# Optimization experiments

Measured on AMD Instinct MI355X. Metric: run time of the kernel, lower is better.

Reference implementation:

```python
import jax, jax.numpy as jnp
import numpy as np

B, S, D = 4, 4096, 1024
H = 8                    # num_heads
DK = D // H              # head_k_dim = 128
DV = D // H              # head_v_dim = 128
KLEPE = 5                # lepe kernel size
ROPE_BASE = 10000.0


def rotate_half(x):
    x1, x2 = jnp.split(x, 2, axis=-1)
    return jnp.concatenate([-x2, x1], axis=-1)


def rope_sin_cos(seq_len, dim):
    inv_freq = 1.0 / (ROPE_BASE ** (jnp.arange(0, dim, 2, dtype=jnp.float32) / dim))
    freqs = jnp.arange(seq_len, dtype=jnp.float32)[:, None] * inv_freq[None, :]
    emb = jnp.concatenate([freqs, freqs], axis=-1)  # [S, dim]
    return jnp.sin(emb), jnp.cos(emb)


def mala_attn(q, k, v):
    """Magnitude-aware linear attention with inline RoPE.

    Attention weights A_ij = (scale*q_i.k_j + 1) / (scale*q_i.(sum_j k_j) + S):
    rows sum to 1 but, unlike plain linear attention, the sharpness of the
    distribution still depends on ||q_i|| (magnitude rectification). Computed
    in O(S*d^2) linear form without materializing the SxS matrix.
    q, k: [B,S,H,DK]; v: [B,S,H,DV].
    """
    sin, cos = rope_sin_cos(q.shape[1], q.shape[-1])
    sin, cos = sin[None, :, None, :], cos[None, :, None, :]
    q = q * cos + rotate_half(q) * sin
    k = k * cos + rotate_half(k) * sin
    scale = q.shape[-1] ** -0.5
    seq_len = q.shape[1]
    kv = jnp.einsum('bshd,bshe->bhde', k, v)      # [B,H,DK,DV]
    ksum = k.sum(axis=1)                          # [B,H,DK]
    vsum = v.sum(axis=1)                          # [B,H,DV]
    num = jnp.einsum('bshd,bhde->bshe', q, kv) * scale + vsum[:, None, :, :]
    den = jnp.einsum('bshd,bhd->bsh', q, ksum) * scale + seq_len
    return num / den[..., None]


def lepe_conv(v, w, b):
    # depthwise Conv1d over the sequence axis; channel id = h*DV + d
    Bb, Ss = v.shape[0], v.shape[1]
    x = v.transpose(0, 2, 3, 1).reshape(Bb, H * DV, Ss)   # [B, C, S]
    y = jax.lax.conv_general_dilated(
        x, w, window_strides=(1,), padding=[(KLEPE // 2, KLEPE // 2)],
        dimension_numbers=('NCH', 'OIH', 'NCH'), feature_group_count=H * DV)
    y = y + b[None, :, None]
    return y.reshape(Bb, H, DV, Ss).transpose(0, 3, 1, 2)  # [B,S,H,DV]


def setup_inputs() -> dict:
    key = jax.random.key(0)
    ks = jax.random.split(key, 8)
    w = 0.02
    return {
        'hidden_states': jax.random.normal(ks[0], (B, S, D), dtype=jnp.float32),
        'Wq': jax.random.normal(ks[1], (D, D), dtype=jnp.float32) * w,
        'Wk': jax.random.normal(ks[2], (D, D), dtype=jnp.float32) * w,
        'Wv': jax.random.normal(ks[3], (D, D), dtype=jnp.float32) * w,
        'Wg': jax.random.normal(ks[4], (D, D), dtype=jnp.float32) * w,
        'Wo': jax.random.normal(ks[5], (D, D), dtype=jnp.float32) * w,
        'lepe_w': jax.random.normal(ks[6], (D, 1, KLEPE), dtype=jnp.float32) * 0.1,
        'lepe_b': jnp.zeros((D,), dtype=jnp.float32),
    }


def reference(hidden_states, Wq, Wk, Wv, Wg, Wo, lepe_w, lepe_b):
    Bb, Ss, _ = hidden_states.shape
    q = (hidden_states @ Wq.T).reshape(Bb, Ss, H, DK)
    k = (hidden_states @ Wk.T).reshape(Bb, Ss, H, DK)
    v = (hidden_states @ Wv.T).reshape(Bb, Ss, H, DV)
    o_gate = hidden_states @ Wg.T                          # [B,S,D]
    o = mala_attn(q, k, v) + lepe_conv(v, lepe_w, lepe_b)  # [B,S,H,DV]
    o = o.reshape(Bb, Ss, H * DV) * o_gate
    return o @ Wo.T
```

## Files before the change

kernel.cpp:

```cpp
#include <hip/hip_runtime.h>
#include <math.h>
#include <stdint.h>


typedef __bf16 bf16;
typedef __bf16 bf16x2 __attribute__((ext_vector_type(2)));
typedef __bf16 bf16x4 __attribute__((ext_vector_type(4)));
typedef __bf16 bf16x8 __attribute__((ext_vector_type(8)));
typedef float f32x4 __attribute__((ext_vector_type(4)));

static constexpr float kScale = 0.08838834764831845f;

__device__ __forceinline__ void async_copy16(const void* g, void* l) {
  __builtin_amdgcn_global_load_lds(
      (const __attribute__((address_space(1))) void*)(uintptr_t)g,
      (__attribute__((address_space(3))) void*)(uintptr_t)l, 16, 0, 0);
}

__global__ __launch_bounds__(512, 1) void gemm_qkvg(
    const bf16* __restrict__ A, const bf16* __restrict__ Bw,
    bf16* __restrict__ C, const float2* __restrict__ tab)
{
  __shared__ __align__(16) char smem[131072];

  const int t = threadIdx.x;
  const int bid = blockIdx.x;
  const int n = bid >> 3;
  const int bx = (bid & 7) * 8 + (n & 7);
  const int by = n >> 3;
  const long m0 = (long)bx * 256;
  const long n0 = (long)by * 256;

  const int d0 = t * 16;
  const int dd = d0 ^ (((d0 >> 7) & 7) << 4);
  const int rT = dd >> 7;
  const int cT = (dd & 127) >> 1;
  const bf16* aSt = A  + (m0 + rT) * 1024 + cT;
  const bf16* bSt = Bw + (n0 + rT) * 1024 + cT;
  char* ldsDst = smem + d0;

  const int lane = t & 63, wid = t >> 6;
  const int wm = wid >> 2, wn = wid & 3;
  const int fm = lane & 15, fq = lane >> 4;
  const int xsw = (fm & 7) << 4;
  const int o0 = (fq * 16) ^ xsw;
  const int o1 = o0 ^ 64;
  const char* ldsA0 = smem + wm * 16384 + fm * 128 + o0;
  const char* ldsA1 = smem + wm * 16384 + fm * 128 + o1;
  const char* ldsB0 = smem + 32768 + (wn >> 1) * 16384 +
                      ((wn & 1) * 64 + fm) * 128 + o0;
  const char* ldsB1 = ldsB0 + (o1 - o0);

  f32x4 acc[8][4] = {};
  bf16x8 a4[4][2], b4[4][2];

#define STAGE_A(kt, h) do {                                                  \
    const bf16* s_ = aSt + (long)(h) * 131072 + (kt) * 64;                   \
    char* d_ = ldsDst + ((kt) & 1) * 65536 + (h) * 16384;                    \
    async_copy16(s_, d_);                                                    \
    async_copy16(s_ + 65536, d_ + 8192);                                     \
  } while (0)
#define STAGE_B(kt, h) do {                                                  \
    const bf16* s_ = bSt + (long)(h) * 131072 + (kt) * 64;                   \
    char* d_ = ldsDst + ((kt) & 1) * 65536 + 32768 + (h) * 16384;            \
    async_copy16(s_, d_);                                                    \
    async_copy16(s_ + 65536, d_ + 8192);                                     \
  } while (0)
#define LOAD_A(buf, qi) do {                                                 \
    const char* p0_ = ldsA0 + (buf) * 65536 + (qi) * 8192;                   \
    const char* p1_ = ldsA1 + (buf) * 65536 + (qi) * 8192;                   \
    a4[0][0] = *(const bf16x8*)(p0_);                                        \
    a4[0][1] = *(const bf16x8*)(p1_);                                        \
    a4[1][0] = *(const bf16x8*)(p0_ + 2048);                                 \
    a4[1][1] = *(const bf16x8*)(p1_ + 2048);                                 \
    a4[2][0] = *(const bf16x8*)(p0_ + 4096);                                 \
    a4[2][1] = *(const bf16x8*)(p1_ + 4096);                                 \
    a4[3][0] = *(const bf16x8*)(p0_ + 6144);                                 \
    a4[3][1] = *(const bf16x8*)(p1_ + 6144);                                 \
  } while (0)
#define LOAD_B(buf, qj) do {                                                 \
    const char* p0_ = ldsB0 + (buf) * 65536 + (qj) * 4096;                   \
    const char* p1_ = ldsB1 + (buf) * 65536 + (qj) * 4096;                   \
    b4[2*(qj)+0][0] = *(const bf16x8*)(p0_);                                 \
    b4[2*(qj)+0][1] = *(const bf16x8*)(p1_);                                 \
    b4[2*(qj)+1][0] = *(const bf16x8*)(p0_ + 2048);                          \
    b4[2*(qj)+1][1] = *(const bf16x8*)(p1_ + 2048);                          \
  } while (0)
#define MM1(i, j, ks)                                                        \
    acc[i][j] = __builtin_amdgcn_mfma_f32_16x16x32_bf16(                     \
        a4[(i) & 3][ks], b4[j][ks], acc[i][j], 0, 0, 0)
#define MFMA_Q(qi, qj) do {                                                  \
    MM1(4*(qi)+0, 2*(qj)+0, 0); MM1(4*(qi)+1, 2*(qj)+0, 0);                  \
    MM1(4*(qi)+2, 2*(qj)+0, 0); MM1(4*(qi)+3, 2*(qj)+0, 0);                  \
    MM1(4*(qi)+0, 2*(qj)+1, 0); MM1(4*(qi)+1, 2*(qj)+1, 0);                  \
    MM1(4*(qi)+2, 2*(qj)+1, 0); MM1(4*(qi)+3, 2*(qj)+1, 0);                  \
    MM1(4*(qi)+0, 2*(qj)+0, 1); MM1(4*(qi)+1, 2*(qj)+0, 1);                  \
    MM1(4*(qi)+2, 2*(qj)+0, 1); MM1(4*(qi)+3, 2*(qj)+0, 1);                  \
    MM1(4*(qi)+0, 2*(qj)+1, 1); MM1(4*(qi)+1, 2*(qj)+1, 1);                  \
    MM1(4*(qi)+2, 2*(qj)+1, 1); MM1(4*(qi)+3, 2*(qj)+1, 1);                  \
  } while (0)
#define BAR()    __builtin_amdgcn_s_barrier()
#define SCHEDB() __builtin_amdgcn_sched_barrier(0)
#define PRIO(p)  __builtin_amdgcn_s_setprio(p)

  STAGE_A(0, 0); STAGE_A(0, 1); STAGE_B(0, 0); STAGE_B(0, 1);
  STAGE_A(1, 0);
  asm volatile("s_waitcnt vmcnt(2)" ::: "memory");
  BAR(); SCHEDB();

#pragma unroll 1
  for (int it = 0; it < 7; ++it) {
    const int k1 = 2 * it + 1;
    const int k2 = 2 * it + 2;
    const int k3 = 2 * it + 3;
    LOAD_A(0, 0); LOAD_B(0, 0);
    STAGE_A(k1, 1);
    BAR(); SCHEDB(); PRIO(1); MFMA_Q(0, 0); PRIO(0); BAR(); SCHEDB();
    LOAD_B(0, 1);
    STAGE_B(k1, 0);
    BAR(); SCHEDB(); PRIO(1); MFMA_Q(0, 1); PRIO(0); BAR(); SCHEDB();
    LOAD_A(0, 1);
    STAGE_B(k1, 1);
    BAR(); SCHEDB(); PRIO(1); MFMA_Q(1, 1); PRIO(0); BAR(); SCHEDB();
    STAGE_A(k2, 0);
    BAR(); SCHEDB(); PRIO(1); MFMA_Q(1, 0); PRIO(0);
    asm volatile("s_waitcnt vmcnt(2)" ::: "memory");
    BAR(); SCHEDB();
    LOAD_A(1, 0); LOAD_B(1, 0);
    STAGE_A(k2, 1);
    BAR(); SCHEDB(); PRIO(1); MFMA_Q(0, 0); PRIO(0); BAR(); SCHEDB();
    LOAD_B(1, 1);
    STAGE_B(k2, 0);
    BAR(); SCHEDB(); PRIO(1); MFMA_Q(0, 1); PRIO(0); BAR(); SCHEDB();
    LOAD_A(1, 1);
    STAGE_B(k2, 1);
    BAR(); SCHEDB(); PRIO(1); MFMA_Q(1, 1); PRIO(0); BAR(); SCHEDB();
    STAGE_A(k3, 0);
    BAR(); SCHEDB(); PRIO(1); MFMA_Q(1, 0); PRIO(0);
    asm volatile("s_waitcnt vmcnt(2)" ::: "memory");
    BAR(); SCHEDB();
  }

  {
    LOAD_A(0, 0); LOAD_B(0, 0);
    STAGE_A(15, 1);
    BAR(); SCHEDB(); PRIO(1); MFMA_Q(0, 0); PRIO(0); BAR(); SCHEDB();
    LOAD_B(0, 1);
    STAGE_B(15, 0);
    BAR(); SCHEDB(); PRIO(1); MFMA_Q(0, 1); PRIO(0); BAR(); SCHEDB();
    LOAD_A(0, 1);
    STAGE_B(15, 1);
    BAR(); SCHEDB(); PRIO(1); MFMA_Q(1, 1); PRIO(0); BAR(); SCHEDB();
    BAR(); SCHEDB(); PRIO(1); MFMA_Q(1, 0); PRIO(0);
    asm volatile("s_waitcnt vmcnt(0)" ::: "memory");
    BAR(); SCHEDB();
    LOAD_A(1, 0); LOAD_B(1, 0);
    BAR(); SCHEDB(); PRIO(1); MFMA_Q(0, 0); PRIO(0); BAR(); SCHEDB();
    LOAD_B(1, 1);
    BAR(); SCHEDB(); PRIO(1); MFMA_Q(0, 1); PRIO(0); BAR(); SCHEDB();
    LOAD_A(1, 1);
    BAR(); SCHEDB(); PRIO(1); MFMA_Q(1, 1); PRIO(0); BAR(); SCHEDB();
    BAR(); SCHEDB(); PRIO(1); MFMA_Q(1, 0); PRIO(0); BAR(); SCHEDB();
  }

#undef STAGE_A
#undef STAGE_B
#undef LOAD_A
#undef LOAD_B
#undef MM1
#undef MFMA_Q
#undef BAR
#undef SCHEDB
#undef PRIO

  bf16* T = (bf16*)smem;
  __syncthreads();
#pragma unroll 1
  for (int hw = 0; hw < 2; ++hw) {
    if (wm == hw) {
#pragma unroll
      for (int rf = 0; rf < 8; ++rf)
#pragma unroll
        for (int cf = 0; cf < 4; ++cf)
#pragma unroll
          for (int r = 0; r < 4; ++r)
            T[(rf * 16 + fq * 4 + r) * 264 + wn * 64 + cf * 16 + fm] =
                (bf16)acc[rf][cf][r];
    }
    __syncthreads();
    if (by < 8) {
#pragma unroll
      for (int ii = 0; ii < 32; ++ii) {
        const int pi = t + ii * 512;
        const int row = pi >> 7, pr = pi & 127;
        const int hd = pr >> 6, i = pr & 63;
        const int c0 = hd * 128 + i;
        const int s = (int)((m0 + hw * 128 + row) & 4095);
        const float2 sc = tab[s * 64 + i];
        float x1 = (float)T[row * 264 + c0];
        float x2 = (float)T[row * 264 + c0 + 64];
        T[row * 264 + c0]      = (bf16)(x1 * sc.y - x2 * sc.x);
        T[row * 264 + c0 + 64] = (bf16)(x2 * sc.y + x1 * sc.x);
      }
      __syncthreads();
    }
#pragma unroll
    for (int ii = 0; ii < 8; ++ii) {
      const int cid = t + ii * 512;
      const int row = cid >> 5, ch = cid & 31;
      *(bf16x8*)(C + (m0 + hw * 128 + row) * 4096 + n0 + ch * 8) =
          *(const bf16x8*)(T + row * 264 + ch * 8);
    }
    __syncthreads();
  }
}

__global__ __launch_bounds__(256, 2) void gemm_final(
    const bf16* __restrict__ A, const bf16* __restrict__ Bw,
    float* __restrict__ C)
{
  __shared__ __align__(16) bf16 As[128 * 32];
  __shared__ __align__(16) bf16 Bs[128 * 32];
  const int t = threadIdx.x;
  const int bid = blockIdx.x;
  const int xcd = bid & 7, n = bid >> 3;
  const int bx = xcd * 16 + (n & 15);
  const int by = n >> 4;
  const long m0 = (long)bx * 128;
  A  += m0 * 1024;
  Bw += (long)by * 131072;
  C  += m0 * 1024 + (long)by * 128;

  const int i0 = t, i1 = t + 256;
  const bf16* gA0 = A  + (long)(i0 >> 2) * 1024 + (i0 & 3) * 8;
  const bf16* gA1 = A  + (long)(i1 >> 2) * 1024 + (i1 & 3) * 8;
  const bf16* gB0 = Bw + (long)(i0 >> 2) * 1024 + (i0 & 3) * 8;
  const bf16* gB1 = Bw + (long)(i1 >> 2) * 1024 + (i1 & 3) * 8;
  bf16* lA0 = As + i0 * 8; bf16* lA1 = As + i1 * 8;
  bf16* lB0 = Bs + i0 * 8; bf16* lB1 = Bs + i1 * 8;

  const int lane = t & 63, wv = t >> 6;
  const int moff = (wv & 1) * 64, noff = (wv >> 1) * 64;
  const int fm = lane & 15, fq = lane >> 4;

  f32x4 acc[4][4] = {};

  for (int k0 = 0; k0 < 1024; k0 += 32) {
    async_copy16(gA0, lA0); async_copy16(gA1, lA1);
    async_copy16(gB0, lB0); async_copy16(gB1, lB1);
    gA0 += 32; gA1 += 32; gB0 += 32; gB1 += 32;
    __syncthreads();
    bf16x8 af[4], bfv[4];
#pragma unroll
    for (int i = 0; i < 4; ++i) {
      af[i]  = *(const bf16x8*)(As + (moff + i * 16 + fm) * 32 + fq * 8);
      bfv[i] = *(const bf16x8*)(Bs + (noff + i * 16 + fm) * 32 + fq * 8);
    }
#pragma unroll
    for (int i = 0; i < 4; ++i)
#pragma unroll
      for (int j = 0; j < 4; ++j)
        acc[i][j] = __builtin_amdgcn_mfma_f32_16x16x32_bf16(af[i], bfv[j], acc[i][j], 0, 0, 0);
    __syncthreads();
  }

#pragma unroll
  for (int i = 0; i < 4; ++i)
#pragma unroll
    for (int j = 0; j < 4; ++j)
#pragma unroll
      for (int r = 0; r < 4; ++r)
        C[(long)(moff + i * 16 + fq * 4 + r) * 1024 + noff + j * 16 + fm] = acc[i][j][r];
}

__global__ __launch_bounds__(256, 2) void gemm_num(
    const bf16* __restrict__ QKVG, const bf16* __restrict__ kvTall,
    const float* __restrict__ ksum, const float* __restrict__ vsum,
    const float* __restrict__ lepe_w, const float* __restrict__ lepe_b,
    bf16* __restrict__ obuf)
{
  __shared__ __align__(16) char smem[17408];
  bf16* As = (bf16*)smem;
  bf16* Bs = (bf16*)(smem + 8192);
  bf16* T  = (bf16*)smem;
  __shared__ float sden[128], svsum[128], slb[128], sksum[128];
  __shared__ float slw[5][128];

  const int t = threadIdx.x;
  const int h = blockIdx.y, b = blockIdx.z;
  const int bh = b * 8 + h;
  const long m0 = (long)blockIdx.x * 128;
  const bf16* A  = QKVG + (long)b * 16777216 + m0 * 4096 + h * 128;
  const bf16* Bw = kvTall + (long)bh * 16384;

  if (t < 128) {
    sksum[t] = ksum[bh * 128 + t];
    svsum[t] = vsum[bh * 128 + t];
    slb[t]   = lepe_b[h * 128 + t];
#pragma unroll
    for (int j = 0; j < 5; ++j) slw[j][t] = lepe_w[(h * 128 + t) * 5 + j];
  }

  const int i0 = t, i1 = t + 256;
  const bf16* gA0 = A + (long)(i0 >> 2) * 4096 + (i0 & 3) * 8;
  const bf16* gA1 = A + (long)(i1 >> 2) * 4096 + (i1 & 3) * 8;
  const bf16* gB0 = Bw + (long)(i0 >> 2) * 128 + (i0 & 3) * 8;
  const bf16* gB1 = Bw + (long)(i1 >> 2) * 128 + (i1 & 3) * 8;
  bf16* lA0 = As + i0 * 8; bf16* lA1 = As + i1 * 8;
  bf16* lB0 = Bs + i0 * 8; bf16* lB1 = Bs + i1 * 8;

  const int lane = t & 63, wv = t >> 6;
  const int moff = (wv & 1) * 64, noff = (wv >> 1) * 64;
  const int fm = lane & 15, fq = lane >> 4;

  f32x4 acc[4][4] = {};
  float dacc = 0.f;

  for (int k0 = 0; k0 < 128; k0 += 32) {
    async_copy16(gA0, lA0); async_copy16(gA1, lA1);
    async_copy16(gB0, lB0); async_copy16(gB1, lB1);
    gA0 += 32; gA1 += 32; gB0 += 32; gB1 += 32;
    __syncthreads();
    bf16x8 af[4], bfv[4];
#pragma unroll
    for (int i = 0; i < 4; ++i) {
      af[i]  = *(const bf16x8*)(As + (moff + i * 16 + fm) * 32 + fq * 8);
      bfv[i] = *(const bf16x8*)(Bs + (noff + i * 16 + fm) * 32 + fq * 8);
    }
#pragma unroll
    for (int i = 0; i < 4; ++i)
#pragma unroll
      for (int j = 0; j < 4; ++j)
        acc[i][j] = __builtin_amdgcn_mfma_f32_16x16x32_bf16(af[i], bfv[j], acc[i][j], 0, 0, 0);
    if (t < 128) {
#pragma unroll
      for (int c8 = 0; c8 < 4; ++c8) {
        bf16x8 q8 = *(const bf16x8*)(As + t * 32 + c8 * 8);
#pragma unroll
        for (int e = 0; e < 8; ++e) dacc += (float)q8[e] * sksum[k0 + c8 * 8 + e];
      }
    }
    __syncthreads();
  }
  if (t < 128) sden[t] = dacc * kScale + 4096.0f;

  const int c2 = lane * 2;
  const float w0[5] = {slw[0][c2], slw[1][c2], slw[2][c2], slw[3][c2], slw[4][c2]};
  const float w1[5] = {slw[0][c2+1], slw[1][c2+1], slw[2][c2+1], slw[3][c2+1], slw[4][c2+1]};
  const float lb0 = slb[c2], lb1 = slb[c2 + 1];

#pragma unroll
  for (int half = 0; half < 2; ++half) {
    if ((wv & 1) == half) {
#pragma unroll
      for (int i = 0; i < 4; ++i)
#pragma unroll
        for (int j = 0; j < 4; ++j)
#pragma unroll
          for (int r = 0; r < 4; ++r) {
            const int col = noff + j * 16 + fm;
            T[(i * 16 + fq * 4 + r) * 136 + col] = (bf16)(acc[i][j][r] * kScale + svsum[col]);
          }
    }
    __syncthreads();
    for (int rr = 0; rr < 16; ++rr) {
      const int lrow = wv * 16 + rr;
      const int row = half * 64 + lrow;
      const int s = (int)(m0 + row);
      const long grow = (long)b * 4096 + s;
      const float rden = 1.0f / sden[row];
      const bf16* vrow = QKVG + grow * 4096 + 2048 + h * 128 + c2;
      bf16x2 a2 = *(const bf16x2*)(T + lrow * 136 + c2);
      float lep0 = lb0, lep1 = lb1;
#pragma unroll
      for (int jt = 0; jt < 5; ++jt) {
        const int srow = s + jt - 2;
        if (srow >= 0 && srow < 4096) {
          bf16x2 v2 = *(const bf16x2*)(vrow + (long)(jt - 2) * 4096);
          lep0 += (float)v2[0] * w0[jt];
          lep1 += (float)v2[1] * w1[jt];
        }
      }
      bf16x2 g2 = *(const bf16x2*)(QKVG + grow * 4096 + 3072 + h * 128 + c2);
      bf16x2 o2;
      o2[0] = (bf16)(((float)a2[0] * rden + lep0) * (float)g2[0]);
      o2[1] = (bf16)(((float)a2[1] * rden + lep1) * (float)g2[1]);
      *(bf16x2*)(obuf + grow * 1024 + h * 128 + c2) = o2;
    }
    __syncthreads();
  }
}

__global__ void prep_kernel(const float* __restrict__ X, const float* __restrict__ Wq,
                            const float* __restrict__ Wk, const float* __restrict__ Wv,
                            const float* __restrict__ Wg, const float* __restrict__ Wo,
                            bf16* __restrict__ Xb, bf16* __restrict__ Wcat,
                            bf16* __restrict__ Wob, float2* __restrict__ tab)
{
  const int blk = blockIdx.x;
  if (blk < 16384) {
    long g = ((long)blk * 256 + threadIdx.x) * 4;
    float4 v = *(const float4*)(X + g);
    bf16x4 o = {(bf16)v.x, (bf16)v.y, (bf16)v.z, (bf16)v.w};
    *(bf16x4*)(Xb + g) = o;
  } else if (blk < 21504) {
    long g = ((long)(blk - 16384) * 256 + threadIdx.x) * 4;
    if (g < 4194304) {
      long idx = g & 1048575;
      int sel = (int)(g >> 20);
      const float* s = sel == 0 ? Wq : sel == 1 ? Wk : sel == 2 ? Wv : Wg;
      float4 v = *(const float4*)(s + idx);
      bf16x4 o = {(bf16)v.x, (bf16)v.y, (bf16)v.z, (bf16)v.w};
      *(bf16x4*)(Wcat + g) = o;
    } else {
      long idx = g - 4194304;
      float4 v = *(const float4*)(Wo + idx);
      bf16x4 o = {(bf16)v.x, (bf16)v.y, (bf16)v.z, (bf16)v.w};
      *(bf16x4*)(Wob + idx) = o;
    }
  } else {
    int idx = (blk - 21504) * 256 + threadIdx.x;
    int s = idx >> 6, i = idx & 63;
    float inv = powf(10000.0f, -((float)(2 * i)) / 128.0f);
    float ang = (float)s * inv;
    float sn, cs;
    sincosf(ang, &sn, &cs);
    tab[idx] = make_float2(sn, cs);
  }
}

__global__ __launch_bounds__(256, 2) void kv_mfma(
    const bf16* __restrict__ QKVG, float* __restrict__ kvp,
    float* __restrict__ ksump, float* __restrict__ vsump)
{
  __shared__ __align__(16) bf16 VT[128 * 40];
  __shared__ __align__(16) bf16 KT[128 * 40];
  const int t = threadIdx.x;
  const int chunk = blockIdx.x, bh = blockIdx.y;
  const int b = bh >> 3, h = bh & 7;
  const long rowbase = ((long)b * 4096 + chunk * 256) * 4096 + h * 128;
  const bf16* Kg = QKVG + rowbase + 1024;
  const bf16* Vg = QKVG + rowbase + 2048;

  const int sp = t >> 4, fc = t & 15;
  const int lane = t & 63, wv = t >> 6;
  const int eoff = (wv & 1) * 64, doff = (wv >> 1) * 64;
  const int fm = lane & 15, fq = lane >> 4;
  const int srow = t & 127;
  const bool sumK = t >= 128;

  f32x4 acc[4][4] = {};
  float rsum = 0.f;

  for (int sb = 0; sb < 256; sb += 32) {
    const long go = (long)(sb + 2 * sp) * 4096 + fc * 8;
    bf16x8 v0 = *(const bf16x8*)(Vg + go);
    bf16x8 v1 = *(const bf16x8*)(Vg + go + 4096);
    bf16x8 k0 = *(const bf16x8*)(Kg + go);
    bf16x8 k1 = *(const bf16x8*)(Kg + go + 4096);
#pragma unroll
    for (int j = 0; j < 8; ++j) {
      const int f = fc * 8 + j;
      bf16x2 vp2 = {v0[j], v1[j]};
      bf16x2 kp2 = {k0[j], k1[j]};
      *(bf16x2*)(VT + f * 40 + 2 * sp) = vp2;
      *(bf16x2*)(KT + f * 40 + 2 * sp) = kp2;
    }
    __syncthreads();
    bf16x8 af[4], bfv[4];
#pragma unroll
    for (int i = 0; i < 4; ++i) {
      af[i]  = *(const bf16x8*)(VT + (eoff + i * 16 + fm) * 40 + fq * 8);
      bfv[i] = *(const bf16x8*)(KT + (doff + i * 16 + fm) * 40 + fq * 8);
    }
#pragma unroll
    for (int i = 0; i < 4; ++i)
#pragma unroll
      for (int j = 0; j < 4; ++j)
        acc[i][j] = __builtin_amdgcn_mfma_f32_16x16x32_bf16(af[i], bfv[j], acc[i][j], 0, 0, 0);
    const bf16* rp = (sumK ? KT : VT) + srow * 40;
#pragma unroll
    for (int i = 0; i < 4; ++i) {
      bf16x8 r8 = *(const bf16x8*)(rp + i * 8);
#pragma unroll
      for (int j = 0; j < 8; ++j) rsum += (float)r8[j];
    }
    __syncthreads();
  }

  float* plane = kvp + ((long)chunk * 32 + bh) * 16384;
#pragma unroll
  for (int i = 0; i < 4; ++i)
#pragma unroll
    for (int j = 0; j < 4; ++j)
#pragma unroll
      for (int r = 0; r < 4; ++r)
        plane[(long)(eoff + i * 16 + fq * 4 + r) * 128 + (doff + j * 16 + fm)] = acc[i][j][r];
  float* sdst = (sumK ? ksump : vsump) + ((long)chunk * 32 + bh) * 128 + srow;
  *sdst = rsum;
}

__global__ void kv_reduce(const float* __restrict__ kvp, const float* __restrict__ ksump,
                          const float* __restrict__ vsump, bf16* __restrict__ kvT,
                          float* __restrict__ ksum, float* __restrict__ vsum)
{
  long g = (long)blockIdx.x * 256 + threadIdx.x;
  long bh = g >> 14, idx = g & 16383;
  float s = 0.f;
#pragma unroll
  for (int c = 0; c < 16; ++c) s += kvp[((long)c * 32 + bh) * 16384 + idx];
  kvT[g] = (bf16)s;
  if (g < 8192) {
    int bh2 = (int)(g >> 8), rem = (int)(g & 255), f = rem & 127;
    const float* src = (rem >> 7) ? ksump : vsump;
    float* dst = (rem >> 7) ? ksum : vsum;
    float s2 = 0.f;
#pragma unroll
    for (int c = 0; c < 16; ++c) s2 += src[((long)c * 32 + bh2) * 128 + f];
    dst[bh2 * 128 + f] = s2;
  }
}

extern "C" void kernel_launch(void* const* d_in, const int* in_sizes, int n_in,
                              void* d_out, int out_size, void* d_ws, size_t ws_size,
                              hipStream_t stream)
{
  const float* X      = (const float*)d_in[0];
  const float* Wq     = (const float*)d_in[1];
  const float* Wk     = (const float*)d_in[2];
  const float* Wv     = (const float*)d_in[3];
  const float* Wg     = (const float*)d_in[4];
  const float* Wo     = (const float*)d_in[5];
  const float* lepe_w = (const float*)d_in[6];
  const float* lepe_b = (const float*)d_in[7];
  float* out = (float*)d_out;

  char* ws = (char*)d_ws;
  bf16*   Xb    = (bf16*)(ws);
  float*  kvp   = (float*)(ws);
  bf16*   Wcat  = (bf16*)(ws + 33554432);
  bf16*   Wob   = (bf16*)(ws + 41943040);
  float2* tab   = (float2*)(ws + 44040192);
  float*  ksump = (float*)(ws + 44040192);
  float*  vsump = (float*)(ws + 44302336);
  bf16*   QKVG  = (bf16*)(ws + 46137344);
  float*  ksum  = (float*)(ws + 180355072);
  float*  vsum  = (float*)(ws + 180371456);
  bf16*   kvT   = (bf16*)(ws + 180387840);
  bf16*   obuf  = (bf16*)(ws + 181960704);

  prep_kernel<<<22528, 256, 0, stream>>>(X, Wq, Wk, Wv, Wg, Wo, Xb, Wcat, Wob, tab);

  gemm_qkvg<<<1024, 512, 0, stream>>>(Xb, Wcat, QKVG, tab);

  kv_mfma<<<dim3(16, 32), 256, 0, stream>>>(QKVG, kvp, ksump, vsump);
  kv_reduce<<<2048, 256, 0, stream>>>(kvp, ksump, vsump, kvT, ksum, vsum);

  gemm_num<<<dim3(32, 8, 4), 256, 0, stream>>>(QKVG, kvT, ksum, vsum, lepe_w, lepe_b, obuf);

  gemm_final<<<1024, 256, 0, stream>>>(obuf, Wob, out);
}
```

Before: 427.4 us.

## Rewrite output projection GEMM with 256x256 tiles and double-buffered pipeline

Replaces the simple 128x128 single-buffered output GEMM with a 256x256-tile, 512-thread kernel. It uses double-buffered async global-to-LDS staging with XOR swizzling, interleaved MFMA quadrants with barriers and priority hints, and an LDS-staged coalesced float4 epilogue. The goal is to raise data reuse and overlap loads with MFMA work, likely mirroring the structure of gemm_qkvg. In exchange, the launch has only 256 blocks, fewer than one wave per CU at most on a 256-CU part, and the kernel depends on hand-tuned waitcnt and barrier ordering.

```diff
diff --git a/kernel.cpp b/kernel.cpp
--- a/kernel.cpp
+++ b/kernel.cpp
@@ -215,62 +215,187 @@
   }
 }
 
-__global__ __launch_bounds__(256, 2) void gemm_final(
+__global__ __launch_bounds__(512, 1) void gemm_final(
     const bf16* __restrict__ A, const bf16* __restrict__ Bw,
     float* __restrict__ C)
 {
-  __shared__ __align__(16) bf16 As[128 * 32];
-  __shared__ __align__(16) bf16 Bs[128 * 32];
+  __shared__ __align__(16) char smem[131072];
+
   const int t = threadIdx.x;
   const int bid = blockIdx.x;
-  const int xcd = bid & 7, n = bid >> 3;
-  const int bx = xcd * 16 + (n & 15);
-  const int by = n >> 4;
-  const long m0 = (long)bx * 128;
-  A  += m0 * 1024;
-  Bw += (long)by * 131072;
-  C  += m0 * 1024 + (long)by * 128;
-
-  const int i0 = t, i1 = t + 256;
-  const bf16* gA0 = A  + (long)(i0 >> 2) * 1024 + (i0 & 3) * 8;
-  const bf16* gA1 = A  + (long)(i1 >> 2) * 1024 + (i1 & 3) * 8;
-  const bf16* gB0 = Bw + (long)(i0 >> 2) * 1024 + (i0 & 3) * 8;
-  const bf16* gB1 = Bw + (long)(i1 >> 2) * 1024 + (i1 & 3) * 8;
-  bf16* lA0 = As + i0 * 8; bf16* lA1 = As + i1 * 8;
-  bf16* lB0 = Bs + i0 * 8; bf16* lB1 = Bs + i1 * 8;
-
-  const int lane = t & 63, wv = t >> 6;
-  const int moff = (wv & 1) * 64, noff = (wv >> 1) * 64;
+  const int n = bid >> 3;
+  const int bx = (bid & 7) * 8 + (n & 7);
+  const int by = n >> 3;
+  const long m0 = (long)bx * 256;
+  const long n0 = (long)by * 256;
+
+  const int d0 = t * 16;
+  const int dd = d0 ^ (((d0 >> 7) & 7) << 4);
+  const int rT = dd >> 7;
+  const int cT = (dd & 127) >> 1;
+  const bf16* aSt = A  + (m0 + rT) * 1024 + cT;
+  const bf16* bSt = Bw + (n0 + rT) * 1024 + cT;
+  char* ldsDst = smem + d0;
+
+  const int lane = t & 63, wid = t >> 6;
+  const int wm = wid >> 2, wn = wid & 3;
   const int fm = lane & 15, fq = lane >> 4;
-
-  f32x4 acc[4][4] = {};
-
-  for (int k0 = 0; k0 < 1024; k0 += 32) {
-    async_copy16(gA0, lA0); async_copy16(gA1, lA1);
-    async_copy16(gB0, lB0); async_copy16(gB1, lB1);
-    gA0 += 32; gA1 += 32; gB0 += 32; gB1 += 32;
-    __syncthreads();
-    bf16x8 af[4], bfv[4];
-#pragma unroll
-    for (int i = 0; i < 4; ++i) {
-      af[i]  = *(const bf16x8*)(As + (moff + i * 16 + fm) * 32 + fq * 8);
-      bfv[i] = *(const bf16x8*)(Bs + (noff + i * 16 + fm) * 32 + fq * 8);
-    }
-#pragma unroll
-    for (int i = 0; i < 4; ++i)
-#pragma unroll
-      for (int j = 0; j < 4; ++j)
-        acc[i][j] = __builtin_amdgcn_mfma_f32_16x16x32_bf16(af[i], bfv[j], acc[i][j], 0, 0, 0);
-    __syncthreads();
-  }
-
-#pragma unroll
-  for (int i = 0; i < 4; ++i)
-#pragma unroll
-    for (int j = 0; j < 4; ++j)
-#pragma unroll
-      for (int r = 0; r < 4; ++r)
-        C[(long)(moff + i * 16 + fq * 4 + r) * 1024 + noff + j * 16 + fm] = acc[i][j][r];
+  const int xsw = (fm & 7) << 4;
+  const int o0 = (fq * 16) ^ xsw;
+  const int o1 = o0 ^ 64;
+  const char* ldsA0 = smem + wm * 16384 + fm * 128 + o0;
+  const char* ldsA1 = smem + wm * 16384 + fm * 128 + o1;
+  const char* ldsB0 = smem + 32768 + (wn >> 1) * 16384 +
+                      ((wn & 1) * 64 + fm) * 128 + o0;
+  const char* ldsB1 = ldsB0 + (o1 - o0);
+
+  f32x4 acc[8][4] = {};
+  bf16x8 a4[4][2], b4[4][2];
+
+#define STAGE_A(kt, h) do {                                                  \
+    const bf16* s_ = aSt + (long)(h) * 131072 + (kt) * 64;                   \
+    char* d_ = ldsDst + ((kt) & 1) * 65536 + (h) * 16384;                    \
+    async_copy16(s_, d_);                                                    \
+    async_copy16(s_ + 65536, d_ + 8192);                                     \
+  } while (0)
+#define STAGE_B(kt, h) do {                                                  \
+    const bf16* s_ = bSt + (long)(h) * 131072 + (kt) * 64;                   \
+    char* d_ = ldsDst + ((kt) & 1) * 65536 + 32768 + (h) * 16384;            \
+    async_copy16(s_, d_);                                                    \
+    async_copy16(s_ + 65536, d_ + 8192);                                     \
+  } while (0)
+#define LOAD_A(buf, qi) do {                                                 \
+    const char* p0_ = ldsA0 + (buf) * 65536 + (qi) * 8192;                   \
+    const char* p1_ = ldsA1 + (buf) * 65536 + (qi) * 8192;                   \
+    a4[0][0] = *(const bf16x8*)(p0_);                                        \
+    a4[0][1] = *(const bf16x8*)(p1_);                                        \
+    a4[1][0] = *(const bf16x8*)(p0_ + 2048);                                 \
+    a4[1][1] = *(const bf16x8*)(p1_ + 2048);                                 \
+    a4[2][0] = *(const bf16x8*)(p0_ + 4096);                                 \
+    a4[2][1] = *(const bf16x8*)(p1_ + 4096);                                 \
+    a4[3][0] = *(const bf16x8*)(p0_ + 6144);                                 \
+    a4[3][1] = *(const bf16x8*)(p1_ + 6144);                                 \
+  } while (0)
+#define LOAD_B(buf, qj) do {                                                 \
+    const char* p0_ = ldsB0 + (buf) * 65536 + (qj) * 4096;                   \
+    const char* p1_ = ldsB1 + (buf) * 65536 + (qj) * 4096;                   \
+    b4[2*(qj)+0][0] = *(const bf16x8*)(p0_);                                 \
+    b4[2*(qj)+0][1] = *(const bf16x8*)(p1_);                                 \
+    b4[2*(qj)+1][0] = *(const bf16x8*)(p0_ + 2048);                          \
+    b4[2*(qj)+1][1] = *(const bf16x8*)(p1_ + 2048);                          \
+  } while (0)
+#define MM1(i, j, ks)                                                        \
+    acc[i][j] = __builtin_amdgcn_mfma_f32_16x16x32_bf16(                     \
+        a4[(i) & 3][ks], b4[j][ks], acc[i][j], 0, 0, 0)
+#define MFMA_Q(qi, qj) do {                                                  \
+    MM1(4*(qi)+0, 2*(qj)+0, 0); MM1(4*(qi)+1, 2*(qj)+0, 0);                  \
+    MM1(4*(qi)+2, 2*(qj)+0, 0); MM1(4*(qi)+3, 2*(qj)+0, 0);                  \
+    MM1(4*(qi)+0, 2*(qj)+1, 0); MM1(4*(qi)+1, 2*(qj)+1, 0);                  \
+    MM1(4*(qi)+2, 2*(qj)+1, 0); MM1(4*(qi)+3, 2*(qj)+1, 0);                  \
+    MM1(4*(qi)+0, 2*(qj)+0, 1); MM1(4*(qi)+1, 2*(qj)+0, 1);                  \
+    MM1(4*(qi)+2, 2*(qj)+0, 1); MM1(4*(qi)+3, 2*(qj)+0, 1);                  \
+    MM1(4*(qi)+0, 2*(qj)+1, 1); MM1(4*(qi)+1, 2*(qj)+1, 1);                  \
+    MM1(4*(qi)+2, 2*(qj)+1, 1); MM1(4*(qi)+3, 2*(qj)+1, 1);                  \
+  } while (0)
+#define BAR()    __builtin_amdgcn_s_barrier()
+#define SCHEDB() __builtin_amdgcn_sched_barrier(0)
+#define PRIO(p)  __builtin_amdgcn_s_setprio(p)
+
+  STAGE_A(0, 0); STAGE_A(0, 1); STAGE_B(0, 0); STAGE_B(0, 1);
+  STAGE_A(1, 0);
+  asm volatile("s_waitcnt vmcnt(2)" ::: "memory");
+  BAR(); SCHEDB();
+
+#pragma unroll 1
+  for (int it = 0; it < 7; ++it) {
+    const int k1 = 2 * it + 1;
+    const int k2 = 2 * it + 2;
+    const int k3 = 2 * it + 3;
+    LOAD_A(0, 0); LOAD_B(0, 0);
+    STAGE_A(k1, 1);
+    BAR(); SCHEDB(); PRIO(1); MFMA_Q(0, 0); PRIO(0); BAR(); SCHEDB();
+    LOAD_B(0, 1);
+    STAGE_B(k1, 0);
+    BAR(); SCHEDB(); PRIO(1); MFMA_Q(0, 1); PRIO(0); BAR(); SCHEDB();
+    LOAD_A(0, 1);
+    STAGE_B(k1, 1);
+    BAR(); SCHEDB(); PRIO(1); MFMA_Q(1, 1); PRIO(0); BAR(); SCHEDB();
+    STAGE_A(k2, 0);
+    BAR(); SCHEDB(); PRIO(1); MFMA_Q(1, 0); PRIO(0);
+    asm volatile("s_waitcnt vmcnt(2)" ::: "memory");
+    BAR(); SCHEDB();
+    LOAD_A(1, 0); LOAD_B(1, 0);
+    STAGE_A(k2, 1);
+    BAR(); SCHEDB(); PRIO(1); MFMA_Q(0, 0); PRIO(0); BAR(); SCHEDB();
+    LOAD_B(1, 1);
+    STAGE_B(k2, 0);
+    BAR(); SCHEDB(); PRIO(1); MFMA_Q(0, 1); PRIO(0); BAR(); SCHEDB();
+    LOAD_A(1, 1);
+    STAGE_B(k2, 1);
+    BAR(); SCHEDB(); PRIO(1); MFMA_Q(1, 1); PRIO(0); BAR(); SCHEDB();
+    STAGE_A(k3, 0);
+    BAR(); SCHEDB(); PRIO(1); MFMA_Q(1, 0); PRIO(0);
+    asm volatile("s_waitcnt vmcnt(2)" ::: "memory");
+    BAR(); SCHEDB();
+  }
+
+  {
+    LOAD_A(0, 0); LOAD_B(0, 0);
+    STAGE_A(15, 1);
+    BAR(); SCHEDB(); PRIO(1); MFMA_Q(0, 0); PRIO(0); BAR(); SCHEDB();
+    LOAD_B(0, 1);
+    STAGE_B(15, 0);
+    BAR(); SCHEDB(); PRIO(1); MFMA_Q(0, 1); PRIO(0); BAR(); SCHEDB();
+    LOAD_A(0, 1);
+    STAGE_B(15, 1);
+    BAR(); SCHEDB(); PRIO(1); MFMA_Q(1, 1); PRIO(0); BAR(); SCHEDB();
+    BAR(); SCHEDB(); PRIO(1); MFMA_Q(1, 0); PRIO(0);
+    asm volatile("s_waitcnt vmcnt(0)" ::: "memory");
+    BAR(); SCHEDB();
+    LOAD_A(1, 0); LOAD_B(1, 0);
+    BAR(); SCHEDB(); PRIO(1); MFMA_Q(0, 0); PRIO(0); BAR(); SCHEDB();
+    LOAD_B(1, 1);
+    BAR(); SCHEDB(); PRIO(1); MFMA_Q(0, 1); PRIO(0); BAR(); SCHEDB();
+    LOAD_A(1, 1);
+    BAR(); SCHEDB(); PRIO(1); MFMA_Q(1, 1); PRIO(0); BAR(); SCHEDB();
+    BAR(); SCHEDB(); PRIO(1); MFMA_Q(1, 0); PRIO(0); BAR(); SCHEDB();
+  }
+
+#undef STAGE_A
+#undef STAGE_B
+#undef LOAD_A
+#undef LOAD_B
+#undef MM1
+#undef MFMA_Q
+#undef BAR
+#undef SCHEDB
+#undef PRIO
+
+  float* T2 = (float*)smem;
+  __syncthreads();
+#pragma unroll 1
+  for (int p = 0; p < 4; ++p) {
+    if (wm == (p >> 1)) {
+      const int rbase = (p & 1) * 4;
+#pragma unroll
+      for (int rf = 0; rf < 4; ++rf)
+#pragma unroll
+        for (int cf = 0; cf < 4; ++cf)
+#pragma unroll
+          for (int r = 0; r < 4; ++r)
+            T2[(rf * 16 + fq * 4 + r) * 260 + wn * 64 + cf * 16 + fm] =
+                acc[rbase + rf][cf][r];
+    }
+    __syncthreads();
+#pragma unroll
+    for (int ii = 0; ii < 8; ++ii) {
+      const int cid = t + ii * 512;
+      const int row = cid >> 6, ch = cid & 63;
+      *(float4*)(C + (m0 + p * 64 + row) * 1024 + n0 + ch * 4) =
+          *(const float4*)(T2 + row * 260 + ch * 4);
+    }
+    __syncthreads();
+  }
 }
 
 __global__ __launch_bounds__(256, 2) void gemm_num(
@@ -558,5 +683,5 @@
 
   gemm_num<<<dim3(32, 8, 4), 256, 0, stream>>>(QKVG, kvT, ksum, vsum, lepe_w, lepe_b, obuf);
 
-  gemm_final<<<1024, 256, 0, stream>>>(obuf, Wob, out);
-}
+  gemm_final<<<256, 512, 0, stream>>>(obuf, Wob, out);
+}
```

After: 494.7 us. 1.16x slower.
